# Kernel optimization log

Hardware: AMD Instinct MI355X
Metric: run time of the kernel (lower is better)

The kernel has to match this reference:

```python
import jax, jax.numpy as jnp
import numpy as np

B, IN, H, OUT, E = 8192, 1024, 4096, 1024, 8
HG = H // 2  # gating hidden

def setup_inputs() -> dict:
    key = jax.random.key(0)
    ks = jax.random.split(key, 9)
    s_in = 1.0 / np.sqrt(IN)
    s_h = 1.0 / np.sqrt(H)
    s_hg = 1.0 / np.sqrt(HG)
    return {
        "x": jax.random.normal(ks[0], (B, IN), jnp.float32),
        # gating MLP: Linear(IN,HG) -> ReLU -> Linear(HG,E) -> softmax
        "gw1": jax.random.uniform(ks[1], (IN, HG), jnp.float32, -s_in, s_in),
        "gb1": jax.random.uniform(ks[2], (HG,), jnp.float32, -s_in, s_in),
        "gw2": jax.random.uniform(ks[3], (HG, E), jnp.float32, -s_hg, s_hg),
        "gb2": jax.random.uniform(ks[4], (E,), jnp.float32, -s_hg, s_hg),
        # experts: E x (Linear(IN,H) -> ReLU -> Linear(H,OUT))
        "ew1": jax.random.uniform(ks[5], (E, IN, H), jnp.float32, -s_in, s_in),
        "eb1": jax.random.uniform(ks[6], (E, H), jnp.float32, -s_in, s_in),
        "ew2": jax.random.uniform(ks[7], (E, H, OUT), jnp.float32, -s_h, s_h),
        "eb2": jax.random.uniform(ks[8], (E, OUT), jnp.float32, -s_h, s_h),
    }

def reference(x, gw1, gb1, gw2, gb2, ew1, eb1, ew2, eb2):
    # Gating network (dropout is a no-op in eval)
    gh = jax.nn.relu(x @ gw1 + gb1)                       # [B, HG]
    gates = jax.nn.softmax(gh @ gw2 + gb2, axis=1)        # [B, E]
    # All experts run on the full batch
    h = jax.nn.relu(jnp.einsum('bi,eih->beh', x, ew1) + eb1[None])  # [B, E, H]
    eo = jnp.einsum('beh,eho->beo', h, ew2) + eb2[None]             # [B, E, OUT]
    # Gate-weighted combine: (stacked * gates[...,None]).sum(dim=1)
    combined = jnp.einsum('beo,be->bo', eo, gates)        # [B, OUT]
    return combined
```

## Files before the change

kernel.cpp:

```cpp
#include <hip/hip_runtime.h>


#define DI __device__ __forceinline__

typedef _Float16 f16;
typedef _Float16 f16x8 __attribute__((ext_vector_type(8)));
typedef float f32x4 __attribute__((ext_vector_type(4)));

constexpr int BSZ  = 8192;
constexpr int IND  = 1024;
constexpr int HID  = 4096;
constexpr int OUTD = 1024;
constexpr int NE   = 8;
constexpr int HGD  = 2048;

__global__ __launch_bounds__(256) void conv_f32_f16_kernel(
    const float* __restrict__ in, f16* __restrict__ out)
{
    size_t i = ((size_t)blockIdx.x * 256 + threadIdx.x) * 8;
    const float4* p = (const float4*)(in + i);
    float4 a = p[0], b = p[1];
    f16x8 v = {(f16)a.x, (f16)a.y, (f16)a.z, (f16)a.w,
               (f16)b.x, (f16)b.y, (f16)b.z, (f16)b.w};
    *(f16x8*)(out + i) = v;
}

__global__ __launch_bounds__(256) void transpose_f32_f16_kernel(
    const float* __restrict__ W, f16* __restrict__ Wt, int K, int N)
{
    __shared__ float t[64][65];
    int n0 = blockIdx.x * 64, k0 = blockIdx.y * 64;
    int tx = threadIdx.x & 63, ty = threadIdx.x >> 6;
#pragma unroll
    for (int i = 0; i < 16; i++) {
        int k = i * 4 + ty;
        t[k][tx] = W[(size_t)(k0 + k) * N + n0 + tx];
    }
    __syncthreads();
#pragma unroll
    for (int i = 0; i < 16; i++) {
        int n = i * 4 + ty;
        Wt[(size_t)(n0 + n) * K + k0 + tx] = (f16)t[tx][n];
    }
}

DI void gload_lds16(const void* g, void* l)
{
    typedef const __attribute__((address_space(1))) unsigned int as1_t;
    typedef __attribute__((address_space(3))) unsigned int as3_t;
    __builtin_amdgcn_global_load_lds(
        (as1_t*)(unsigned long long)(__SIZE_TYPE__)g,
        (as3_t*)(unsigned int)(__SIZE_TYPE__)l,
        16, 0, 0);
}


#define VMAIN { if constexpr (NBC == 2) asm volatile("s_waitcnt vmcnt(8)");   \
                else                     asm volatile("s_waitcnt vmcnt(6)"); }
#define VMTAIL1 { if constexpr (NBC == 2) asm volatile("s_waitcnt vmcnt(4)"); \
                  else                     asm volatile("s_waitcnt vmcnt(3)"); }
#define VMTAIL2 { asm volatile("s_waitcnt vmcnt(0)"); }

#define STG(TT, BB) { stA(BB, 0, TT); stA(BB, 1, TT); stB(BB, 0, TT);         \
                      if constexpr (NBC == 2) stB(BB, 1, TT); }

#define PHASE(B, STAGE, VM)                                                    \
  {                                                                            \
    f16x8 av[8]; f16x8 bv[NF];                                                 \
    _Pragma("unroll") for (int f = 0; f < 8; f++)                              \
        av[f] = *(const f16x8*)(sAc + (B) * 16384 + offA[f]);                  \
    _Pragma("unroll") for (int n = 0; n < NF; n++)                             \
        bv[n] = *(const f16x8*)(sBc + (B) * (BN * 64) + offB[n]);              \
    STAGE                                                                      \
    __builtin_amdgcn_sched_barrier(0);                                         \
    __builtin_amdgcn_s_barrier();                                              \
    asm volatile("s_waitcnt lgkmcnt(0)" ::: "memory");                         \
    __builtin_amdgcn_sched_barrier(0);                                         \
    __builtin_amdgcn_s_setprio(1);                                             \
    _Pragma("unroll") for (int fm = 0; fm < 8; fm++)                           \
      _Pragma("unroll") for (int n = 0; n < NF; n++)                           \
        acc[fm][n] = __builtin_amdgcn_mfma_f32_16x16x32_f16(                   \
            av[fm], bv[n], acc[fm][n], 0, 0, 0);                               \
    __builtin_amdgcn_s_setprio(0);                                             \
    VM                                                                         \
    __builtin_amdgcn_sched_barrier(0);                                         \
    __builtin_amdgcn_s_barrier();                                              \
    asm volatile("" ::: "memory");                                             \
  }

template <int BN, bool RELU, bool GATE, bool OUT_F16, bool ACCUM>
__global__ __launch_bounds__(512, 2) void gemm4b_kernel(
    const f16* __restrict__ A, const f16* __restrict__ Bt,
    const float* __restrict__ bias, const float* __restrict__ gate,
    void* __restrict__ Cptr, int M, int N, int K)
{
    constexpr int BM = 256, BK = 32;
    constexpr int NF  = BN / 64;
    constexpr int NBC = BN / 128;
    __shared__ __align__(16) f16 sA[4][BM * BK];
    __shared__ __align__(16) f16 sB[4][BN * BK];
    const char* sAc = (const char*)&sA[0][0];
    const char* sBc = (const char*)&sB[0][0];

    const int tid = threadIdx.x, wid = tid >> 6, lane = tid & 63;
    const int wm = wid >> 2, wn = wid & 3;

    const int nwg = gridDim.x, bid = blockIdx.x;
    const int wg  = (bid & 7) * (nwg >> 3) + (bid >> 3);
    const int gx  = N / BN;
    const size_t bm = (size_t)(wg / gx) * BM;
    const size_t bn = (size_t)(wg % gx) * BN;

    f32x4 acc[8][NF] = {};

    const int sP   = tid >> 3;
    const int offp = (((tid >> 2) & 1) << 6) | ((tid & 3) << 4);
    const int offl = offp ^ ((sP & 7) << 4);
    const int srow = (sP << 1) | (offl >> 6);
    const int skel = (offl & 63) >> 1;
    const f16* pA = A  + (bm + srow) * (size_t)K + skel;
    const f16* pB = Bt + (bn + srow) * (size_t)K + skel;

    auto stA = [&](int b, int q, int T) {
        gload_lds16(pA + (size_t)(q * 128) * K + (size_t)T * BK,
                    (char*)sAc + b * 16384 + q * 8192 + wid * 1024);
    };
    auto stB = [&](int b, int q, int T) {
        gload_lds16(pB + (size_t)(q * 128) * K + (size_t)T * BK,
                    (char*)sBc + b * (BN * 64) + q * 8192 + wid * 1024);
    };

    int offA[8], offB[NF];
    const int ks4 = (lane >> 4) << 4;
#pragma unroll
    for (int f = 0; f < 8; f++) {
        int r = wm * 128 + f * 16 + (lane & 15);
        int s = r >> 1;
        offA[f] = s * 128 + ((((r & 1) << 6) | ks4) ^ ((s & 7) << 4));
    }
#pragma unroll
    for (int n = 0; n < NF; n++) {
        int r = wn * (BN / 4) + n * 16 + (lane & 15);
        int s = r >> 1;
        offB[n] = s * 128 + ((((r & 1) << 6) | ks4) ^ ((s & 7) << 4));
    }

    const int NT = K / BK, NI = NT / 4;

    STG(0, 0) STG(1, 1) STG(2, 2)
    if constexpr (NBC == 2) { asm volatile("s_waitcnt vmcnt(8)"); }
    else                    { asm volatile("s_waitcnt vmcnt(6)"); }
    __builtin_amdgcn_s_barrier();
    asm volatile("" ::: "memory");

    for (int i = 0; i < NI - 1; ++i) {
        const int T = 4 * i;
        PHASE(0, STG(T + 3, 3), VMAIN)
        PHASE(1, STG(T + 4, 0), VMAIN)
        PHASE(2, STG(T + 5, 1), VMAIN)
        PHASE(3, STG(T + 6, 2), VMAIN)
    }
    {
        const int T = NT - 4;
        PHASE(0, STG(T + 3, 3), VMAIN)
        PHASE(1, {}, VMTAIL1)
        PHASE(2, {}, VMTAIL2)
        PHASE(3, {}, {})
    }

    const size_t row0 = bm + (size_t)wm * 128;
    const int col0 = (int)bn + wn * (BN / 4);
    const int c0 = lane & 15, r0 = (lane >> 4) * 4;
#pragma unroll
    for (int fm = 0; fm < 8; fm++) {
#pragma unroll
        for (int r = 0; r < 4; r++) {
            const size_t row = row0 + fm * 16 + r0 + r;
            float g = 1.0f;
            if constexpr (GATE) g = gate[row * NE];
#pragma unroll
            for (int n = 0; n < NF; n++) {
                const size_t col = (size_t)col0 + n * 16 + c0;
                float v = acc[fm][n][r] + bias[col];
                if constexpr (RELU) v = fmaxf(v, 0.0f);
                if constexpr (GATE) v *= g;
                if constexpr (OUT_F16) {
                    ((f16*)Cptr)[row * (size_t)N + col] = (f16)v;
                } else {
                    float* p = (float*)Cptr + row * (size_t)N + col;
                    *p = ACCUM ? (*p + v) : v;
                }
            }
        }
    }
}

__global__ __launch_bounds__(256) void gate_softmax_kernel(
    const f16* __restrict__ gh, const float* __restrict__ gw2,
    const float* __restrict__ gb2, float* __restrict__ gates)
{
    const int row  = blockIdx.x * 4 + (threadIdx.x >> 6);
    const int lane = threadIdx.x & 63;
    const f16* r = gh + (size_t)row * HGD;
    float acc[NE] = {};
    for (int k = lane; k < HGD; k += 64) {
        float h = (float)r[k];
        const float* w = gw2 + (size_t)k * NE;
#pragma unroll
        for (int e = 0; e < NE; e++) acc[e] = fmaf(h, w[e], acc[e]);
    }
#pragma unroll
    for (int off = 32; off > 0; off >>= 1)
#pragma unroll
        for (int e = 0; e < NE; e++) acc[e] += __shfl_down(acc[e], off, 64);
    if (lane == 0) {
        float l[NE], m = -1e30f;
#pragma unroll
        for (int e = 0; e < NE; e++) { l[e] = acc[e] + gb2[e]; m = fmaxf(m, l[e]); }
        float s = 0.f;
#pragma unroll
        for (int e = 0; e < NE; e++) { l[e] = expf(l[e] - m); s += l[e]; }
        float inv = 1.0f / s;
#pragma unroll
        for (int e = 0; e < NE; e++) gates[(size_t)row * NE + e] = l[e] * inv;
    }
}

extern "C" void kernel_launch(void* const* d_in, const int* in_sizes, int n_in,
                              void* d_out, int out_size, void* d_ws, size_t ws_size,
                              hipStream_t stream)
{
    const float* x   = (const float*)d_in[0];
    const float* gw1 = (const float*)d_in[1];
    const float* gb1 = (const float*)d_in[2];
    const float* gw2 = (const float*)d_in[3];
    const float* gb2 = (const float*)d_in[4];
    const float* ew1 = (const float*)d_in[5];
    const float* eb1 = (const float*)d_in[6];
    const float* ew2 = (const float*)d_in[7];
    const float* eb2 = (const float*)d_in[8];
    float* out = (float*)d_out;

    char* ws = (char*)d_ws;
    float* gates = (float*)ws;
    f16* x16  = (f16*)(ws + (256 << 10));
    f16* wbuf = x16 + (size_t)BSZ * IND;
    f16* hbuf = wbuf + (size_t)HID * IND;
    f16* gh   = hbuf;

    conv_f32_f16_kernel<<<(BSZ * IND) / (256 * 8), 256, 0, stream>>>(x, x16);

    transpose_f32_f16_kernel<<<dim3(HGD / 64, IND / 64), 256, 0, stream>>>(gw1, wbuf, IND, HGD);
    gemm4b_kernel<256, true, false, true, false>
        <<<(HGD / 256) * (BSZ / 256), 512, 0, stream>>>(
            x16, wbuf, gb1, nullptr, gh, BSZ, HGD, IND);

    gate_softmax_kernel<<<BSZ / 4, 256, 0, stream>>>(gh, gw2, gb2, gates);

    for (int e = 0; e < NE; e++) {
        transpose_f32_f16_kernel<<<dim3(HID / 64, IND / 64), 256, 0, stream>>>(
            ew1 + (size_t)e * IND * HID, wbuf, IND, HID);
        gemm4b_kernel<256, true, false, true, false>
            <<<(HID / 256) * (BSZ / 256), 512, 0, stream>>>(
                x16, wbuf, eb1 + (size_t)e * HID, nullptr, hbuf, BSZ, HID, IND);

        transpose_f32_f16_kernel<<<dim3(OUTD / 64, HID / 64), 256, 0, stream>>>(
            ew2 + (size_t)e * HID * OUTD, wbuf, HID, OUTD);
        if (e == 0)
            gemm4b_kernel<128, false, true, false, false>
                <<<(OUTD / 128) * (BSZ / 256), 512, 0, stream>>>(
                    hbuf, wbuf, eb2 + (size_t)e * OUTD, gates + e, out, BSZ, OUTD, HID);
        else
            gemm4b_kernel<128, false, true, false, true>
                <<<(OUTD / 128) * (BSZ / 256), 512, 0, stream>>>(
                    hbuf, wbuf, eb2 + (size_t)e * OUTD, gates + e, out, BSZ, OUTD, HID);
    }
}
```

Baseline: 1.433 ms.

## Restructure GEMM pipeline to BK=64 double-buffered quadrant-interleaved MFMA schedule

Replaces the generic 4-stage BK=32 GEMM with two specialized kernels that use BK=64 tiles in a double buffer. Each K-tile is split into quadrant or octant MFMA phases, with global-to-LDS loads for the next tile interleaved between them. The aim is fewer barriers per unit of MFMA work and better overlap of loads with compute. In exchange the code is much more complex, the waitcnt and barrier bookkeeping is fragile, and LDS use per block changes.

```diff
diff --git a/kernel.cpp b/kernel.cpp
--- a/kernel.cpp
+++ b/kernel.cpp
@@ -54,145 +54,372 @@
         16, 0, 0);
 }
 
-
-#define VMAIN { if constexpr (NBC == 2) asm volatile("s_waitcnt vmcnt(8)");   \
-                else                     asm volatile("s_waitcnt vmcnt(6)"); }
-#define VMTAIL1 { if constexpr (NBC == 2) asm volatile("s_waitcnt vmcnt(4)"); \
-                  else                     asm volatile("s_waitcnt vmcnt(3)"); }
-#define VMTAIL2 { asm volatile("s_waitcnt vmcnt(0)"); }
-
-#define STG(TT, BB) { stA(BB, 0, TT); stA(BB, 1, TT); stB(BB, 0, TT);         \
-                      if constexpr (NBC == 2) stB(BB, 1, TT); }
-
-#define PHASE(B, STAGE, VM)                                                    \
-  {                                                                            \
-    f16x8 av[8]; f16x8 bv[NF];                                                 \
-    _Pragma("unroll") for (int f = 0; f < 8; f++)                              \
-        av[f] = *(const f16x8*)(sAc + (B) * 16384 + offA[f]);                  \
-    _Pragma("unroll") for (int n = 0; n < NF; n++)                             \
-        bv[n] = *(const f16x8*)(sBc + (B) * (BN * 64) + offB[n]);              \
-    STAGE                                                                      \
+#define SYNC_HEAD                                                              \
     __builtin_amdgcn_sched_barrier(0);                                         \
     __builtin_amdgcn_s_barrier();                                              \
     asm volatile("s_waitcnt lgkmcnt(0)" ::: "memory");                         \
+    __builtin_amdgcn_sched_barrier(0);
+#define SYNC_HEAD_T8                                                           \
     __builtin_amdgcn_sched_barrier(0);                                         \
-    __builtin_amdgcn_s_setprio(1);                                             \
-    _Pragma("unroll") for (int fm = 0; fm < 8; fm++)                           \
-      _Pragma("unroll") for (int n = 0; n < NF; n++)                           \
-        acc[fm][n] = __builtin_amdgcn_mfma_f32_16x16x32_f16(                   \
-            av[fm], bv[n], acc[fm][n], 0, 0, 0);                               \
-    __builtin_amdgcn_s_setprio(0);                                             \
-    VM                                                                         \
+    asm volatile("s_waitcnt lgkmcnt(8)");                                      \
+    __builtin_amdgcn_s_barrier();                                              \
+    asm volatile("s_waitcnt lgkmcnt(0)" ::: "memory");                         \
+    __builtin_amdgcn_sched_barrier(0);
+#define SYNC_TAIL                                                              \
     __builtin_amdgcn_sched_barrier(0);                                         \
     __builtin_amdgcn_s_barrier();                                              \
-    asm volatile("" ::: "memory");                                             \
-  }
-
-template <int BN, bool RELU, bool GATE, bool OUT_F16, bool ACCUM>
-__global__ __launch_bounds__(512, 2) void gemm4b_kernel(
+    asm volatile("" ::: "memory");
+
+template <bool RELU>
+__global__ __launch_bounds__(512, 2) void gemm256_kernel(
     const f16* __restrict__ A, const f16* __restrict__ Bt,
-    const float* __restrict__ bias, const float* __restrict__ gate,
-    void* __restrict__ Cptr, int M, int N, int K)
-{
-    constexpr int BM = 256, BK = 32;
-    constexpr int NF  = BN / 64;
-    constexpr int NBC = BN / 128;
-    __shared__ __align__(16) f16 sA[4][BM * BK];
-    __shared__ __align__(16) f16 sB[4][BN * BK];
-    const char* sAc = (const char*)&sA[0][0];
-    const char* sBc = (const char*)&sB[0][0];
+    const float* __restrict__ bias, f16* __restrict__ Cptr,
+    int M, int N, int K)
+{
+    constexpr int BM = 256, BN = 256, BK = 64;
+    constexpr int AT = BM * BK * 2, BT = BN * BK * 2;
+    __shared__ __align__(16) f16 sA[2][BM * BK];
+    __shared__ __align__(16) f16 sB[2][BN * BK];
+    const char* sAc = (const char*)sA;
+    const char* sBc = (const char*)sB;
 
     const int tid = threadIdx.x, wid = tid >> 6, lane = tid & 63;
     const int wm = wid >> 2, wn = wid & 3;
-
     const int nwg = gridDim.x, bid = blockIdx.x;
-    const int wg  = (bid & 7) * (nwg >> 3) + (bid >> 3);
-    const int gx  = N / BN;
+    const int wg = (bid & 7) * (nwg >> 3) + (bid >> 3);
+    const int gx = N / BN;
     const size_t bm = (size_t)(wg / gx) * BM;
     const size_t bn = (size_t)(wg % gx) * BN;
 
-    f32x4 acc[8][NF] = {};
-
-    const int sP   = tid >> 3;
-    const int offp = (((tid >> 2) & 1) << 6) | ((tid & 3) << 4);
-    const int offl = offp ^ ((sP & 7) << 4);
-    const int srow = (sP << 1) | (offl >> 6);
-    const int skel = (offl & 63) >> 1;
-    const f16* pA = A  + (bm + srow) * (size_t)K + skel;
-    const f16* pB = Bt + (bn + srow) * (size_t)K + skel;
+    f32x4 acc[8][4] = {};
+
+    const int rho  = tid >> 3;
+    const int slot = (((tid & 7) << 4) ^ (((tid >> 3) & 7) << 4));
+    const f16* pA = A  + (bm + rho) * (size_t)K + (slot >> 1);
+    const f16* pB = Bt + (bn + rho) * (size_t)K + (slot >> 1);
 
     auto stA = [&](int b, int q, int T) {
-        gload_lds16(pA + (size_t)(q * 128) * K + (size_t)T * BK,
-                    (char*)sAc + b * 16384 + q * 8192 + wid * 1024);
+        gload_lds16(pA + ((size_t)q * 64) * K + (size_t)T * BK,
+                    (char*)sAc + b * AT + q * 8192 + wid * 1024);
     };
     auto stB = [&](int b, int q, int T) {
-        gload_lds16(pB + (size_t)(q * 128) * K + (size_t)T * BK,
-                    (char*)sBc + b * (BN * 64) + q * 8192 + wid * 1024);
+        gload_lds16(pB + ((size_t)q * 64) * K + (size_t)T * BK,
+                    (char*)sBc + b * BT + q * 8192 + wid * 1024);
     };
 
-    int offA[8], offB[NF];
-    const int ks4 = (lane >> 4) << 4;
+    int offA0[8], offB0[4];
 #pragma unroll
     for (int f = 0; f < 8; f++) {
         int r = wm * 128 + f * 16 + (lane & 15);
-        int s = r >> 1;
-        offA[f] = s * 128 + ((((r & 1) << 6) | ks4) ^ ((s & 7) << 4));
-    }
-#pragma unroll
-    for (int n = 0; n < NF; n++) {
-        int r = wn * (BN / 4) + n * 16 + (lane & 15);
-        int s = r >> 1;
-        offB[n] = s * 128 + ((((r & 1) << 6) | ks4) ^ ((s & 7) << 4));
-    }
-
-    const int NT = K / BK, NI = NT / 4;
-
-    STG(0, 0) STG(1, 1) STG(2, 2)
-    if constexpr (NBC == 2) { asm volatile("s_waitcnt vmcnt(8)"); }
-    else                    { asm volatile("s_waitcnt vmcnt(6)"); }
+        offA0[f] = r * 128 + ((((lane >> 4) << 4)) ^ ((r & 7) << 4));
+    }
+#pragma unroll
+    for (int f = 0; f < 4; f++) {
+        int r = wn * 64 + f * 16 + (lane & 15);
+        offB0[f] = r * 128 + ((((lane >> 4) << 4)) ^ ((r & 7) << 4));
+    }
+
+    f16x8 av[4][2], bv0[2][2], bv1[2][2];
+
+#define LDAQ(B, MH)                                                            \
+    _Pragma("unroll") for (int f = 0; f < 4; f++)                              \
+    _Pragma("unroll") for (int kc = 0; kc < 2; kc++)                           \
+        av[f][kc] = *(const f16x8*)(sAc + (B) * AT + (offA0[(MH)*4+f] ^ (kc << 6)));
+#define LDBH(B, NH, BV)                                                        \
+    _Pragma("unroll") for (int f = 0; f < 2; f++)                              \
+    _Pragma("unroll") for (int kc = 0; kc < 2; kc++)                           \
+        BV[f][kc] = *(const f16x8*)(sBc + (B) * BT + (offB0[(NH)*2+f] ^ (kc << 6)));
+#define QUAD(MH, NH, BV)                                                       \
+    __builtin_amdgcn_s_setprio(1);                                             \
+    _Pragma("unroll") for (int f = 0; f < 4; f++)                              \
+    _Pragma("unroll") for (int g = 0; g < 2; g++)                              \
+    _Pragma("unroll") for (int kc = 0; kc < 2; kc++)                           \
+        acc[(MH)*4+f][(NH)*2+g] = __builtin_amdgcn_mfma_f32_16x16x32_f16(      \
+            av[f][kc], BV[g][kc], acc[(MH)*4+f][(NH)*2+g], 0, 0, 0);           \
+    __builtin_amdgcn_s_setprio(0);
+
+    const int NT = K / BK, NI = NT / 2;
+
+    stA(0,0,0); stA(0,2,0); stB(0,0,0); stB(0,1,0); stB(0,2,0); stB(0,3,0);
+    stA(0,1,0); stA(0,3,0);
+    stA(1,0,1); stA(1,2,1); stB(1,0,1); stB(1,1,1); stB(1,2,1); stB(1,3,1);
+    asm volatile("s_waitcnt vmcnt(6)");
     __builtin_amdgcn_s_barrier();
     asm volatile("" ::: "memory");
 
     for (int i = 0; i < NI - 1; ++i) {
-        const int T = 4 * i;
-        PHASE(0, STG(T + 3, 3), VMAIN)
-        PHASE(1, STG(T + 4, 0), VMAIN)
-        PHASE(2, STG(T + 5, 1), VMAIN)
-        PHASE(3, STG(T + 6, 2), VMAIN)
+        const int t = 2 * i;
+        LDAQ(0, 0) LDBH(0, 0, bv0)
+        stA(1, 1, t + 1); stA(1, 3, t + 1);
+        SYNC_HEAD_T8
+        QUAD(0, 0, bv0)
+        SYNC_TAIL
+        LDBH(0, 1, bv1)
+        stA(0, 0, t + 2); stA(0, 2, t + 2);
+        SYNC_HEAD
+        QUAD(0, 1, bv1)
+        SYNC_TAIL
+        LDAQ(0, 1)
+        stB(0, 0, t + 2); stB(0, 1, t + 2);
+        SYNC_HEAD
+        QUAD(1, 1, bv1)
+        SYNC_TAIL
+        stB(0, 2, t + 2); stB(0, 3, t + 2);
+        SYNC_HEAD
+        QUAD(1, 0, bv0)
+        asm volatile("s_waitcnt vmcnt(6)");
+        SYNC_TAIL
+        LDAQ(1, 0) LDBH(1, 0, bv0)
+        stA(0, 1, t + 2); stA(0, 3, t + 2);
+        SYNC_HEAD_T8
+        QUAD(0, 0, bv0)
+        SYNC_TAIL
+        LDBH(1, 1, bv1)
+        stA(1, 0, t + 3); stA(1, 2, t + 3);
+        SYNC_HEAD
+        QUAD(0, 1, bv1)
+        SYNC_TAIL
+        LDAQ(1, 1)
+        stB(1, 0, t + 3); stB(1, 1, t + 3);
+        SYNC_HEAD
+        QUAD(1, 1, bv1)
+        SYNC_TAIL
+        stB(1, 2, t + 3); stB(1, 3, t + 3);
+        SYNC_HEAD
+        QUAD(1, 0, bv0)
+        asm volatile("s_waitcnt vmcnt(6)");
+        SYNC_TAIL
     }
     {
-        const int T = NT - 4;
-        PHASE(0, STG(T + 3, 3), VMAIN)
-        PHASE(1, {}, VMTAIL1)
-        PHASE(2, {}, VMTAIL2)
-        PHASE(3, {}, {})
-    }
+        LDAQ(0, 0) LDBH(0, 0, bv0)
+        stA(1, 1, NT - 1); stA(1, 3, NT - 1);
+        SYNC_HEAD_T8
+        QUAD(0, 0, bv0)
+        SYNC_TAIL
+        LDBH(0, 1, bv1)
+        SYNC_HEAD
+        QUAD(0, 1, bv1)
+        SYNC_TAIL
+        LDAQ(0, 1)
+        SYNC_HEAD
+        QUAD(1, 1, bv1)
+        SYNC_TAIL
+        SYNC_HEAD
+        QUAD(1, 0, bv0)
+        asm volatile("s_waitcnt vmcnt(0)");
+        SYNC_TAIL
+        LDAQ(1, 0) LDBH(1, 0, bv0)
+        SYNC_HEAD
+        QUAD(0, 0, bv0)
+        SYNC_TAIL
+        LDBH(1, 1, bv1)
+        SYNC_HEAD
+        QUAD(0, 1, bv1)
+        SYNC_TAIL
+        LDAQ(1, 1)
+        SYNC_HEAD
+        QUAD(1, 1, bv1)
+        SYNC_TAIL
+        SYNC_HEAD
+        QUAD(1, 0, bv0)
+        SYNC_TAIL
+    }
+#undef LDAQ
+#undef LDBH
+#undef QUAD
 
     const size_t row0 = bm + (size_t)wm * 128;
-    const int col0 = (int)bn + wn * (BN / 4);
+    const int col0 = (int)bn + wn * 64;
     const int c0 = lane & 15, r0 = (lane >> 4) * 4;
 #pragma unroll
-    for (int fm = 0; fm < 8; fm++) {
+    for (int fm = 0; fm < 8; fm++)
 #pragma unroll
         for (int r = 0; r < 4; r++) {
             const size_t row = row0 + fm * 16 + r0 + r;
-            float g = 1.0f;
-            if constexpr (GATE) g = gate[row * NE];
-#pragma unroll
-            for (int n = 0; n < NF; n++) {
+#pragma unroll
+            for (int n = 0; n < 4; n++) {
                 const size_t col = (size_t)col0 + n * 16 + c0;
                 float v = acc[fm][n][r] + bias[col];
                 if constexpr (RELU) v = fmaxf(v, 0.0f);
-                if constexpr (GATE) v *= g;
-                if constexpr (OUT_F16) {
-                    ((f16*)Cptr)[row * (size_t)N + col] = (f16)v;
-                } else {
-                    float* p = (float*)Cptr + row * (size_t)N + col;
-                    *p = ACCUM ? (*p + v) : v;
-                }
+                Cptr[row * (size_t)N + col] = (f16)v;
             }
         }
-    }
+}
+
+template <bool ACCUM>
+__global__ __launch_bounds__(512, 2) void gemmO_kernel(
+    const f16* __restrict__ A, const f16* __restrict__ Bt,
+    const float* __restrict__ bias, const float* __restrict__ gate,
+    float* __restrict__ Cptr, int M, int N, int K)
+{
+    constexpr int BM = 256, BN = 128, BK = 64;
+    constexpr int AT = BM * BK * 2, BT = BN * BK * 2;
+    __shared__ __align__(16) f16 sA[2][BM * BK];
+    __shared__ __align__(16) f16 sB[2][BN * BK];
+    const char* sAc = (const char*)sA;
+    const char* sBc = (const char*)sB;
+
+    const int tid = threadIdx.x, wid = tid >> 6, lane = tid & 63;
+    const int wm = wid >> 2, wn = wid & 3;
+    const int nwg = gridDim.x, bid = blockIdx.x;
+    const int wg = (bid & 7) * (nwg >> 3) + (bid >> 3);
+    const int gx = N / BN;
+    const size_t bm = (size_t)(wg / gx) * BM;
+    const size_t bn = (size_t)(wg % gx) * BN;
+
+    f32x4 acc[8][2] = {};
+
+    const int rho  = tid >> 3;
+    const int slot = (((tid & 7) << 4) ^ (((tid >> 3) & 7) << 4));
+    const f16* pA = A  + (bm + rho) * (size_t)K + (slot >> 1);
+    const f16* pB = Bt + (bn + rho) * (size_t)K + (slot >> 1);
+
+    auto stA = [&](int b, int q, int T) {
+        gload_lds16(pA + ((size_t)q * 64) * K + (size_t)T * BK,
+                    (char*)sAc + b * AT + q * 8192 + wid * 1024);
+    };
+    auto stB = [&](int b, int q, int T) {
+        gload_lds16(pB + ((size_t)q * 64) * K + (size_t)T * BK,
+                    (char*)sBc + b * BT + q * 8192 + wid * 1024);
+    };
+
+    int offA0[8], offB0[2];
+#pragma unroll
+    for (int f = 0; f < 8; f++) {
+        int r = wm * 128 + f * 16 + (lane & 15);
+        offA0[f] = r * 128 + ((((lane >> 4) << 4)) ^ ((r & 7) << 4));
+    }
+#pragma unroll
+    for (int f = 0; f < 2; f++) {
+        int r = wn * 32 + f * 16 + (lane & 15);
+        offB0[f] = r * 128 + ((((lane >> 4) << 4)) ^ ((r & 7) << 4));
+    }
+
+    f16x8 av[4], bv[2][2];
+
+#define LDA4(B, MH, KC)                                                        \
+    _Pragma("unroll") for (int f = 0; f < 4; f++)                              \
+        av[f] = *(const f16x8*)(sAc + (B) * AT + (offA0[(MH)*4+f] ^ ((KC) << 6)));
+#define LDBA(B)                                                                \
+    _Pragma("unroll") for (int f = 0; f < 2; f++)                              \
+    _Pragma("unroll") for (int kc = 0; kc < 2; kc++)                           \
+        bv[f][kc] = *(const f16x8*)(sBc + (B) * BT + (offB0[f] ^ (kc << 6)));
+#define OCT(MH, KC)                                                            \
+    __builtin_amdgcn_s_setprio(1);                                             \
+    _Pragma("unroll") for (int f = 0; f < 4; f++)                              \
+    _Pragma("unroll") for (int g = 0; g < 2; g++)                              \
+        acc[(MH)*4+f][g] = __builtin_amdgcn_mfma_f32_16x16x32_f16(             \
+            av[f], bv[g][KC], acc[(MH)*4+f][g], 0, 0, 0);                      \
+    __builtin_amdgcn_s_setprio(0);
+
+    const int NT = K / BK, NI = NT / 2;
+
+    stA(0,0,0); stA(0,2,0); stB(0,0,0); stB(0,1,0); stA(0,1,0); stA(0,3,0);
+    stA(1,0,1); stA(1,2,1); stB(1,0,1); stB(1,1,1);
+    asm volatile("s_waitcnt vmcnt(4)");
+    __builtin_amdgcn_s_barrier();
+    asm volatile("" ::: "memory");
+
+    for (int i = 0; i < NI - 1; ++i) {
+        const int t = 2 * i;
+        LDA4(0, 0, 0) LDBA(0)
+        stA(1, 1, t + 1); stA(1, 3, t + 1);
+        SYNC_HEAD
+        OCT(0, 0)
+        SYNC_TAIL
+        LDA4(0, 0, 1)
+        SYNC_HEAD
+        OCT(0, 1)
+        SYNC_TAIL
+        LDA4(0, 1, 0)
+        stA(0, 0, t + 2); stA(0, 2, t + 2);
+        SYNC_HEAD
+        OCT(1, 0)
+        SYNC_TAIL
+        LDA4(0, 1, 1)
+        stB(0, 0, t + 2); stB(0, 1, t + 2);
+        SYNC_HEAD
+        OCT(1, 1)
+        asm volatile("s_waitcnt vmcnt(4)");
+        SYNC_TAIL
+        LDA4(1, 0, 0) LDBA(1)
+        stA(0, 1, t + 2); stA(0, 3, t + 2);
+        SYNC_HEAD
+        OCT(0, 0)
+        SYNC_TAIL
+        LDA4(1, 0, 1)
+        SYNC_HEAD
+        OCT(0, 1)
+        SYNC_TAIL
+        LDA4(1, 1, 0)
+        stA(1, 0, t + 3); stA(1, 2, t + 3);
+        SYNC_HEAD
+        OCT(1, 0)
+        SYNC_TAIL
+        LDA4(1, 1, 1)
+        stB(1, 0, t + 3); stB(1, 1, t + 3);
+        SYNC_HEAD
+        OCT(1, 1)
+        asm volatile("s_waitcnt vmcnt(4)");
+        SYNC_TAIL
+    }
+    {
+        LDA4(0, 0, 0) LDBA(0)
+        stA(1, 1, NT - 1); stA(1, 3, NT - 1);
+        SYNC_HEAD
+        OCT(0, 0)
+        SYNC_TAIL
+        LDA4(0, 0, 1)
+        SYNC_HEAD
+        OCT(0, 1)
+        SYNC_TAIL
+        LDA4(0, 1, 0)
+        SYNC_HEAD
+        OCT(1, 0)
+        SYNC_TAIL
+        LDA4(0, 1, 1)
+        SYNC_HEAD
+        OCT(1, 1)
+        asm volatile("s_waitcnt vmcnt(0)");
+        SYNC_TAIL
+        LDA4(1, 0, 0) LDBA(1)
+        SYNC_HEAD
+        OCT(0, 0)
+        SYNC_TAIL
+        LDA4(1, 0, 1)
+        SYNC_HEAD
+        OCT(0, 1)
+        SYNC_TAIL
+        LDA4(1, 1, 0)
+        SYNC_HEAD
+        OCT(1, 0)
+        SYNC_TAIL
+        LDA4(1, 1, 1)
+        SYNC_HEAD
+        OCT(1, 1)
+        SYNC_TAIL
+    }
+#undef LDA4
+#undef LDBA
+#undef OCT
+
+    const size_t row0 = bm + (size_t)wm * 128;
+    const int col0 = (int)bn + wn * 32;
+    const int c0 = lane & 15, r0 = (lane >> 4) * 4;
+#pragma unroll
+    for (int fm = 0; fm < 8; fm++)
+#pragma unroll
+        for (int r = 0; r < 4; r++) {
+            const size_t row = row0 + fm * 16 + r0 + r;
+            const float g = gate[row * NE];
+#pragma unroll
+            for (int n = 0; n < 2; n++) {
+                const size_t col = (size_t)col0 + n * 16 + c0;
+                float v = (acc[fm][n][r] + bias[col]) * g;
+                float* p = Cptr + row * (size_t)N + col;
+                *p = ACCUM ? (*p + v) : v;
+            }
+        }
 }
 
 __global__ __launch_bounds__(256) void gate_softmax_kernel(
@@ -251,27 +478,27 @@
     conv_f32_f16_kernel<<<(BSZ * IND) / (256 * 8), 256, 0, stream>>>(x, x16);
 
     transpose_f32_f16_kernel<<<dim3(HGD / 64, IND / 64), 256, 0, stream>>>(gw1, wbuf, IND, HGD);
-    gemm4b_kernel<256, true, false, true, false>
+    gemm256_kernel<true>
         <<<(HGD / 256) * (BSZ / 256), 512, 0, stream>>>(
-            x16, wbuf, gb1, nullptr, gh, BSZ, HGD, IND);
+            x16, wbuf, gb1, gh, BSZ, HGD, IND);
 
     gate_softmax_kernel<<<BSZ / 4, 256, 0, stream>>>(gh, gw2, gb2, gates);
 
     for (int e = 0; e < NE; e++) {
         transpose_f32_f16_kernel<<<dim3(HID / 64, IND / 64), 256, 0, stream>>>(
             ew1 + (size_t)e * IND * HID, wbuf, IND, HID);
-        gemm4b_kernel<256, true, false, true, false>
+        gemm256_kernel<true>
             <<<(HID / 256) * (BSZ / 256), 512, 0, stream>>>(
-                x16, wbuf, eb1 + (size_t)e * HID, nullptr, hbuf, BSZ, HID, IND);
+                x16, wbuf, eb1 + (size_t)e * HID, hbuf, BSZ, HID, IND);
 
         transpose_f32_f16_kernel<<<dim3(OUTD / 64, HID / 64), 256, 0, stream>>>(
             ew2 + (size_t)e * HID * OUTD, wbuf, HID, OUTD);
         if (e == 0)
-            gemm4b_kernel<128, false, true, false, false>
+            gemmO_kernel<false>
                 <<<(OUTD / 128) * (BSZ / 256), 512, 0, stream>>>(
                     hbuf, wbuf, eb2 + (size_t)e * OUTD, gates + e, out, BSZ, OUTD, HID);
         else
-            gemm4b_kernel<128, false, true, false, true>
+            gemmO_kernel<true>
                 <<<(OUTD / 128) * (BSZ / 256), 512, 0, stream>>>(
                     hbuf, wbuf, eb2 + (size_t)e * OUTD, gates + e, out, BSZ, OUTD, HID);
     }
```

Result: faster. 1.381 ms (-3.7%).

## Replace 4-stage BK=32 GEMM with 3-stage BK=64 split-phase pipeline

Applied to the files above, without the earlier changes.

Rewrites the MFMA GEMM to use BK=64 tiles with a triple-buffered LDS ring. Each k-tile is split into two half-M phases, with A and B global-to-LDS loads staggered across the phases. The first-layer GEMMs drop from BN=256 to BN=128, which doubles the grid and removes the templated BN. The aim is to cut barriers per K step and overlap loads better, at the cost of less reuse per block in the first layer and trickier vmcnt/lgkmcnt bookkeeping.

```diff
diff --git a/kernel.cpp b/kernel.cpp
--- a/kernel.cpp
+++ b/kernel.cpp
@@ -54,122 +54,139 @@
         16, 0, 0);
 }
 
-
-#define VMAIN { if constexpr (NBC == 2) asm volatile("s_waitcnt vmcnt(8)");   \
-                else                     asm volatile("s_waitcnt vmcnt(6)"); }
-#define VMTAIL1 { if constexpr (NBC == 2) asm volatile("s_waitcnt vmcnt(4)"); \
-                  else                     asm volatile("s_waitcnt vmcnt(3)"); }
-#define VMTAIL2 { asm volatile("s_waitcnt vmcnt(0)"); }
-
-#define STG(TT, BB) { stA(BB, 0, TT); stA(BB, 1, TT); stB(BB, 0, TT);         \
-                      if constexpr (NBC == 2) stB(BB, 1, TT); }
-
-#define PHASE(B, STAGE, VM)                                                    \
-  {                                                                            \
-    f16x8 av[8]; f16x8 bv[NF];                                                 \
-    _Pragma("unroll") for (int f = 0; f < 8; f++)                              \
-        av[f] = *(const f16x8*)(sAc + (B) * 16384 + offA[f]);                  \
-    _Pragma("unroll") for (int n = 0; n < NF; n++)                             \
-        bv[n] = *(const f16x8*)(sBc + (B) * (BN * 64) + offB[n]);              \
-    STAGE                                                                      \
+#define SYNC_HEAD                                                              \
     __builtin_amdgcn_sched_barrier(0);                                         \
     __builtin_amdgcn_s_barrier();                                              \
     asm volatile("s_waitcnt lgkmcnt(0)" ::: "memory");                         \
+    __builtin_amdgcn_sched_barrier(0);
+#define SYNC_HEAD_T8                                                           \
     __builtin_amdgcn_sched_barrier(0);                                         \
-    __builtin_amdgcn_s_setprio(1);                                             \
-    _Pragma("unroll") for (int fm = 0; fm < 8; fm++)                           \
-      _Pragma("unroll") for (int n = 0; n < NF; n++)                           \
-        acc[fm][n] = __builtin_amdgcn_mfma_f32_16x16x32_f16(                   \
-            av[fm], bv[n], acc[fm][n], 0, 0, 0);                               \
-    __builtin_amdgcn_s_setprio(0);                                             \
-    VM                                                                         \
+    asm volatile("s_waitcnt lgkmcnt(8)");                                      \
+    __builtin_amdgcn_s_barrier();                                              \
+    asm volatile("s_waitcnt lgkmcnt(0)" ::: "memory");                         \
+    __builtin_amdgcn_sched_barrier(0);
+#define SYNC_TAIL                                                              \
     __builtin_amdgcn_sched_barrier(0);                                         \
     __builtin_amdgcn_s_barrier();                                              \
-    asm volatile("" ::: "memory");                                             \
+    asm volatile("" ::: "memory");
+
+
+#define PHA(B, T)                                                              \
+  {                                                                            \
+    _Pragma("unroll") for (int f = 0; f < 4; f++)                              \
+    _Pragma("unroll") for (int kc = 0; kc < 2; kc++)                           \
+        av[f][kc] = *(const f16x8*)(sAc + (B) * ATILE + (offA0[f] ^ (kc << 6))); \
+    _Pragma("unroll") for (int g = 0; g < 2; g++)                              \
+    _Pragma("unroll") for (int kc = 0; kc < 2; kc++)                           \
+        bv[g][kc] = *(const f16x8*)(sBc + (B) * BTILE + (offB0[g] ^ (kc << 6))); \
+    if ((T) + 2 < NT) {                                                        \
+        stA(((B) + 2) % 3, 0, (T) + 2); stA(((B) + 2) % 3, 1, (T) + 2);        \
+        stA(((B) + 2) % 3, 2, (T) + 2); stA(((B) + 2) % 3, 3, (T) + 2);        \
+    }                                                                          \
+    SYNC_HEAD_T8                                                               \
+    __builtin_amdgcn_s_setprio(1);                                             \
+    _Pragma("unroll") for (int f = 0; f < 4; f++)                              \
+    _Pragma("unroll") for (int g = 0; g < 2; g++)                              \
+    _Pragma("unroll") for (int kc = 0; kc < 2; kc++)                           \
+        acc[f][g] = __builtin_amdgcn_mfma_f32_16x16x32_f16(                    \
+            av[f][kc], bv[g][kc], acc[f][g], 0, 0, 0);                         \
+    __builtin_amdgcn_s_setprio(0);                                             \
+    SYNC_TAIL                                                                  \
   }
 
-template <int BN, bool RELU, bool GATE, bool OUT_F16, bool ACCUM>
-__global__ __launch_bounds__(512, 2) void gemm4b_kernel(
+#define PHB(B, T)                                                              \
+  {                                                                            \
+    _Pragma("unroll") for (int f = 0; f < 4; f++)                              \
+    _Pragma("unroll") for (int kc = 0; kc < 2; kc++)                           \
+        av[f][kc] = *(const f16x8*)(sAc + (B) * ATILE + 8192 + (offA0[f] ^ (kc << 6))); \
+    if ((T) + 3 < NT) { stB((B), 0, (T) + 3); stB((B), 1, (T) + 3); }          \
+    SYNC_HEAD                                                                  \
+    __builtin_amdgcn_s_setprio(1);                                             \
+    _Pragma("unroll") for (int f = 0; f < 4; f++)                              \
+    _Pragma("unroll") for (int g = 0; g < 2; g++)                              \
+    _Pragma("unroll") for (int kc = 0; kc < 2; kc++)                           \
+        acc[4 + f][g] = __builtin_amdgcn_mfma_f32_16x16x32_f16(                \
+            av[f][kc], bv[g][kc], acc[4 + f][g], 0, 0, 0);                     \
+    __builtin_amdgcn_s_setprio(0);                                             \
+    if ((T) <= NT - 4)      { asm volatile("s_waitcnt vmcnt(8)"); }            \
+    else if ((T) == NT - 3) { asm volatile("s_waitcnt vmcnt(6)"); }            \
+    else if ((T) == NT - 2) { asm volatile("s_waitcnt vmcnt(0)"); }            \
+    SYNC_TAIL                                                                  \
+  }
+
+template <bool RELU, bool GATE, bool OUT_F16, bool ACCUM>
+__global__ __launch_bounds__(512, 2) void gemm3b_kernel(
     const f16* __restrict__ A, const f16* __restrict__ Bt,
     const float* __restrict__ bias, const float* __restrict__ gate,
     void* __restrict__ Cptr, int M, int N, int K)
 {
-    constexpr int BM = 256, BK = 32;
-    constexpr int NF  = BN / 64;
-    constexpr int NBC = BN / 128;
-    __shared__ __align__(16) f16 sA[4][BM * BK];
-    __shared__ __align__(16) f16 sB[4][BN * BK];
-    const char* sAc = (const char*)&sA[0][0];
-    const char* sBc = (const char*)&sB[0][0];
+    constexpr int BM = 256, BN = 128, BK = 64;
+    constexpr int ATILE = BM * BK * 2;
+    constexpr int BTILE = BN * BK * 2;
+    __shared__ __align__(16) f16 sA[3][BM * BK];
+    __shared__ __align__(16) f16 sB[3][BN * BK];
+    const char* sAc = (const char*)sA;
+    const char* sBc = (const char*)sB;
 
     const int tid = threadIdx.x, wid = tid >> 6, lane = tid & 63;
     const int wm = wid >> 2, wn = wid & 3;
 
     const int nwg = gridDim.x, bid = blockIdx.x;
-    const int wg  = (bid & 7) * (nwg >> 3) + (bid >> 3);
-    const int gx  = N / BN;
+    const int wg = (bid & 7) * (nwg >> 3) + (bid >> 3);
+    const int gx = N / BN;
     const size_t bm = (size_t)(wg / gx) * BM;
     const size_t bn = (size_t)(wg % gx) * BN;
 
-    f32x4 acc[8][NF] = {};
-
-    const int sP   = tid >> 3;
-    const int offp = (((tid >> 2) & 1) << 6) | ((tid & 3) << 4);
-    const int offl = offp ^ ((sP & 7) << 4);
-    const int srow = (sP << 1) | (offl >> 6);
-    const int skel = (offl & 63) >> 1;
-    const f16* pA = A  + (bm + srow) * (size_t)K + skel;
-    const f16* pB = Bt + (bn + srow) * (size_t)K + skel;
+    f32x4 acc[8][2] = {};
+
+    const int rho  = tid >> 3;
+    const int slot = (((tid & 7) << 4) ^ (((tid >> 3) & 7) << 4));
+    const f16* pA = A  + (bm + rho) * (size_t)K + (slot >> 1);
+    const f16* pB = Bt + (bn + rho) * (size_t)K + (slot >> 1);
 
     auto stA = [&](int b, int q, int T) {
-        gload_lds16(pA + (size_t)(q * 128) * K + (size_t)T * BK,
-                    (char*)sAc + b * 16384 + q * 8192 + wid * 1024);
+        gload_lds16(pA + ((size_t)q * 64) * K + (size_t)T * BK,
+                    (char*)sAc + b * ATILE + q * 8192 + wid * 1024);
     };
     auto stB = [&](int b, int q, int T) {
-        gload_lds16(pB + (size_t)(q * 128) * K + (size_t)T * BK,
-                    (char*)sBc + b * (BN * 64) + q * 8192 + wid * 1024);
+        gload_lds16(pB + ((size_t)q * 64) * K + (size_t)T * BK,
+                    (char*)sBc + b * BTILE + q * 8192 + wid * 1024);
     };
 
-    int offA[8], offB[NF];
+    int offA0[4], offB0[2];
     const int ks4 = (lane >> 4) << 4;
 #pragma unroll
-    for (int f = 0; f < 8; f++) {
+    for (int f = 0; f < 4; f++) {
         int r = wm * 128 + f * 16 + (lane & 15);
-        int s = r >> 1;
-        offA[f] = s * 128 + ((((r & 1) << 6) | ks4) ^ ((s & 7) << 4));
-    }
-#pragma unroll
-    for (int n = 0; n < NF; n++) {
-        int r = wn * (BN / 4) + n * 16 + (lane & 15);
-        int s = r >> 1;
-        offB[n] = s * 128 + ((((r & 1) << 6) | ks4) ^ ((s & 7) << 4));
-    }
-
-    const int NT = K / BK, NI = NT / 4;
-
-    STG(0, 0) STG(1, 1) STG(2, 2)
-    if constexpr (NBC == 2) { asm volatile("s_waitcnt vmcnt(8)"); }
-    else                    { asm volatile("s_waitcnt vmcnt(6)"); }
+        offA0[f] = r * 128 + (ks4 ^ ((r & 7) << 4));
+    }
+#pragma unroll
+    for (int g = 0; g < 2; g++) {
+        int r = wn * 32 + g * 16 + (lane & 15);
+        offB0[g] = r * 128 + (ks4 ^ ((r & 7) << 4));
+    }
+
+    f16x8 av[4][2], bv[2][2];
+    const int NT = K / BK;
+
+    stA(0, 0, 0); stA(0, 1, 0); stA(0, 2, 0); stA(0, 3, 0);
+    stB(0, 0, 0); stB(0, 1, 0);
+    stA(1, 0, 1); stA(1, 1, 1); stA(1, 2, 1); stA(1, 3, 1);
+    stB(1, 0, 1); stB(1, 1, 1);
+    stB(2, 0, 2); stB(2, 1, 2);
+    asm volatile("s_waitcnt vmcnt(8)");
     __builtin_amdgcn_s_barrier();
     asm volatile("" ::: "memory");
 
-    for (int i = 0; i < NI - 1; ++i) {
-        const int T = 4 * i;
-        PHASE(0, STG(T + 3, 3), VMAIN)
-        PHASE(1, STG(T + 4, 0), VMAIN)
-        PHASE(2, STG(T + 5, 1), VMAIN)
-        PHASE(3, STG(T + 6, 2), VMAIN)
-    }
-    {
-        const int T = NT - 4;
-        PHASE(0, STG(T + 3, 3), VMAIN)
-        PHASE(1, {}, VMTAIL1)
-        PHASE(2, {}, VMTAIL2)
-        PHASE(3, {}, {})
+    PHA(0, 0) PHB(0, 0)
+    for (int t = 1; t < NT; t += 3) {
+        PHA(1, t)     PHB(1, t)
+        PHA(2, t + 1) PHB(2, t + 1)
+        PHA(0, t + 2) PHB(0, t + 2)
     }
 
     const size_t row0 = bm + (size_t)wm * 128;
-    const int col0 = (int)bn + wn * (BN / 4);
+    const int col0 = (int)bn + wn * 32;
     const int c0 = lane & 15, r0 = (lane >> 4) * 4;
 #pragma unroll
     for (int fm = 0; fm < 8; fm++) {
@@ -179,7 +196,7 @@
             float g = 1.0f;
             if constexpr (GATE) g = gate[row * NE];
 #pragma unroll
-            for (int n = 0; n < NF; n++) {
+            for (int n = 0; n < 2; n++) {
                 const size_t col = (size_t)col0 + n * 16 + c0;
                 float v = acc[fm][n][r] + bias[col];
                 if constexpr (RELU) v = fmaxf(v, 0.0f);
@@ -251,8 +268,8 @@
     conv_f32_f16_kernel<<<(BSZ * IND) / (256 * 8), 256, 0, stream>>>(x, x16);
 
     transpose_f32_f16_kernel<<<dim3(HGD / 64, IND / 64), 256, 0, stream>>>(gw1, wbuf, IND, HGD);
-    gemm4b_kernel<256, true, false, true, false>
-        <<<(HGD / 256) * (BSZ / 256), 512, 0, stream>>>(
+    gemm3b_kernel<true, false, true, false>
+        <<<(HGD / 128) * (BSZ / 256), 512, 0, stream>>>(
             x16, wbuf, gb1, nullptr, gh, BSZ, HGD, IND);
 
     gate_softmax_kernel<<<BSZ / 4, 256, 0, stream>>>(gh, gw2, gb2, gates);
@@ -260,18 +277,18 @@
     for (int e = 0; e < NE; e++) {
         transpose_f32_f16_kernel<<<dim3(HID / 64, IND / 64), 256, 0, stream>>>(
             ew1 + (size_t)e * IND * HID, wbuf, IND, HID);
-        gemm4b_kernel<256, true, false, true, false>
-            <<<(HID / 256) * (BSZ / 256), 512, 0, stream>>>(
+        gemm3b_kernel<true, false, true, false>
+            <<<(HID / 128) * (BSZ / 256), 512, 0, stream>>>(
                 x16, wbuf, eb1 + (size_t)e * HID, nullptr, hbuf, BSZ, HID, IND);
 
         transpose_f32_f16_kernel<<<dim3(OUTD / 64, HID / 64), 256, 0, stream>>>(
             ew2 + (size_t)e * HID * OUTD, wbuf, HID, OUTD);
         if (e == 0)
-            gemm4b_kernel<128, false, true, false, false>
+            gemm3b_kernel<false, true, false, false>
                 <<<(OUTD / 128) * (BSZ / 256), 512, 0, stream>>>(
                     hbuf, wbuf, eb2 + (size_t)e * OUTD, gates + e, out, BSZ, OUTD, HID);
         else
-            gemm4b_kernel<128, false, true, false, true>
+            gemm3b_kernel<false, true, false, true>
                 <<<(OUTD / 128) * (BSZ / 256), 512, 0, stream>>>(
                     hbuf, wbuf, eb2 + (size_t)e * OUTD, gates + e, out, BSZ, OUTD, HID);
     }
```

Result: slower. 1.576 ms (+10.0%).
